# Kernel tuning notes

Measured on AMD Instinct MI355X. Metric: run time of the kernel, lower is better.

## Reference

```python
import jax, jax.numpy as jnp
import numpy as np

IN_CH = 128
OUT_CH = 256
KSIZE = 3
DOWN = 2
WSCALE_GAIN = 1.0
LR_MUL = 1.0
ACT_GAIN = float(np.sqrt(2.0))  # lrelu def_gain
CONV_CLAMP = 256.0
LRELU_SLOPE = 0.2


def _setup_filter():
    # upfirdn2d.setup_filter([1,3,3,1]): normalize 1D then outer product -> 2D
    f1 = jnp.asarray([1.0, 3.0, 3.0, 1.0], dtype=jnp.float32)
    f1 = f1 / jnp.sum(f1)
    f2 = jnp.outer(f1, f1)  # [4,4]
    return f2


def setup_inputs() -> dict:
    key = jax.random.key(0)
    k1, k2 = jax.random.split(key)
    x = jax.random.normal(k1, (16, IN_CH, 256, 256), dtype=jnp.float32)
    weight = jax.random.normal(k2, (OUT_CH, IN_CH, KSIZE, KSIZE), dtype=jnp.float32)
    bias = jnp.zeros((OUT_CH,), dtype=jnp.float32)
    return {"x": x, "weight": weight, "bias": bias}


def reference(x, weight, bias):
    # runtime_gain = 1.0
    fan_in = KSIZE * KSIZE * IN_CH
    wscale = WSCALE_GAIN / np.sqrt(fan_in) * LR_MUL  # use_wscale=True
    w = weight * jnp.float32(wscale)
    b = bias * jnp.float32(LR_MUL)

    # filter_padding for k=3, fh=fw=4, down=2 -> (2,2,2,2) as (left,right,top,bottom)
    pad = (KSIZE // 2 + (4 - DOWN + 1) // 2, KSIZE // 2 + (4 - DOWN) // 2)
    # upfirdn2d(x, f, down=1, padding): pad then correlate with flipped filter
    f2 = _setup_filter()
    f2 = f2[::-1, ::-1]  # flip (symmetric here, kept for faithfulness)
    C = x.shape[1]
    fk = jnp.broadcast_to(f2[None, None], (C, 1, 4, 4))  # depthwise kernel
    x = lax.pad_fn(x, pad) if False else jnp.pad(x, ((0, 0), (0, 0), (pad[1], pad[0]) if False else (pad[0], pad[1]), (pad[0], pad[1])))
    x = jax.lax.conv_general_dilated(
        x, fk, window_strides=(1, 1), padding='VALID',
        dimension_numbers=('NCHW', 'OIHW', 'NCHW'),
        feature_group_count=C)

    # strided conv2d, padding=0, stride=down
    x = jax.lax.conv_general_dilated(
        x, w, window_strides=(DOWN, DOWN), padding='VALID',
        dimension_numbers=('NCHW', 'OIHW', 'NCHW'))

    # fused bias + lrelu + gain + clamp
    x = x + b[None, :, None, None]
    x = jnp.where(x >= 0, x, x * jnp.float32(LRELU_SLOPE)) * jnp.float32(ACT_GAIN)
    x = jnp.clip(x, -jnp.float32(CONV_CLAMP), jnp.float32(CONV_CLAMP))
    return x
```

## Files before the change

### kernel.cpp

```cpp
#include <hip/hip_runtime.h>

typedef __attribute__((ext_vector_type(8))) short bf16x8;
typedef __attribute__((ext_vector_type(4))) float f32x4;
typedef __attribute__((ext_vector_type(2))) float f32x2;
typedef __attribute__((ext_vector_type(4))) unsigned int u32x4;

static __device__ __forceinline__ unsigned short f2bf(float f) {
    union { float f; unsigned u; } v; v.f = f;
    return (unsigned short)((v.u + 0x7FFFu + ((v.u >> 16) & 1u)) >> 16);
}

static __device__ __forceinline__ void g2l16(const void* g, void* l) {
    __builtin_amdgcn_global_load_lds(
        (const __attribute__((address_space(1))) unsigned int*)g,
        (__attribute__((address_space(3))) unsigned int*)l, 16, 0, 0);
}

__global__ void prep_weights(const float* __restrict__ w, unsigned short* __restrict__ wp) {
    int t = blockIdx.x * 256 + threadIdx.x;
    const float wscale = 0.02946278254943948f;
    int cw = t & 31;
    int oc = (t >> 5) & 255;
    int cr = t >> 13;
    int ch = cr / 9;
    int rs = cr - ch * 9;
    int r  = rs / 3;
    int s  = rs - r * 3;
    int c  = ch * 32 + cw;
    wp[t] = f2bf(w[((oc * 128 + c) * 3 + r) * 3 + s] * wscale);
}

#define BPX(ROW) {                                                             \
    int _xr = xr0 + (ROW);                                                     \
    int _xc = _xr < 0 ? 0 : (_xr > 255 ? 255 : _xr);                           \
    float _rm = (_xr == _xc) ? 0.125f : 0.0f;                                  \
    const float* _p0 = pq0 + (_xc << 8);                                       \
    const float* _p1 = pq1 + (_xc << 8);                                       \
    f32x4 _l0, _l1; f32x2 _h0, _h1;                                            \
    __builtin_memcpy(&_l0, _p0, 16); __builtin_memcpy(&_h0, _p0 + 4, 8);       \
    __builtin_memcpy(&_l1, _p1, 16); __builtin_memcpy(&_h1, _p1 + 4, 8);       \
    hA0[(ROW) & 3] = (_l0.x + 3.f * (_l0.y + _l0.z) + _l0.w) * _rm;            \
    hB0[(ROW) & 3] = (_l0.y + 3.f * (_l0.z + _l0.w) + _h0.x) * _rm;            \
    hC0[(ROW) & 3] = (_l0.z + 3.f * (_l0.w + _h0.x) + _h0.y) * _rm;            \
    hA1[(ROW) & 3] = (_l1.x + 3.f * (_l1.y + _l1.z) + _l1.w) * _rm;            \
    hB1[(ROW) & 3] = (_l1.y + 3.f * (_l1.z + _l1.w) + _h1.x) * _rm;            \
    hC1[(ROW) & 3] = (_l1.z + 3.f * (_l1.w + _h1.x) + _h1.y) * _rm;            \
}
#define BPS(ROW) {                                                             \
    int _xr = xr0 + (ROW);                                                     \
    float a0=0.f,a1=0.f,a2=0.f,a3=0.f,a4=0.f,a5=0.f;                           \
    float b0=0.f,b1=0.f,b2=0.f,b3=0.f,b4=0.f,b5=0.f;                           \
    if ((unsigned)_xr < 256u) {                                                \
        const float* _p0 = pq0 + (_xr << 8);                                   \
        const float* _p1 = pq1 + (_xr << 8);                                   \
        if ((unsigned)(wc + 0) < 256u) { a0 = _p0[0]; b0 = _p1[0]; }           \
        if ((unsigned)(wc + 1) < 256u) { a1 = _p0[1]; b1 = _p1[1]; }           \
        if ((unsigned)(wc + 2) < 256u) { a2 = _p0[2]; b2 = _p1[2]; }           \
        if ((unsigned)(wc + 3) < 256u) { a3 = _p0[3]; b3 = _p1[3]; }           \
        if ((unsigned)(wc + 4) < 256u) { a4 = _p0[4]; b4 = _p1[4]; }           \
        if ((unsigned)(wc + 5) < 256u) { a5 = _p0[5]; b5 = _p1[5]; }           \
    }                                                                          \
    hA0[(ROW) & 3] = (a0 + 3.f * (a1 + a2) + a3) * 0.125f;                     \
    hB0[(ROW) & 3] = (a1 + 3.f * (a2 + a3) + a4) * 0.125f;                     \
    hC0[(ROW) & 3] = (a2 + 3.f * (a3 + a4) + a5) * 0.125f;                     \
    hA1[(ROW) & 3] = (b0 + 3.f * (b1 + b2) + b3) * 0.125f;                     \
    hB1[(ROW) & 3] = (b1 + 3.f * (b2 + b3) + b4) * 0.125f;                     \
    hC1[(ROW) & 3] = (b2 + 3.f * (b3 + b4) + b5) * 0.125f;                     \
}
#define BPV(ROW) {                                                             \
    float vA0 = (hA0[(ROW-3)&3] + 3.f*(hA0[(ROW-2)&3]+hA0[(ROW-1)&3]) + hA0[(ROW)&3]) * 0.125f; \
    float vA1 = (hA1[(ROW-3)&3] + 3.f*(hA1[(ROW-2)&3]+hA1[(ROW-1)&3]) + hA1[(ROW)&3]) * 0.125f; \
    float vB0 = (hB0[(ROW-3)&3] + 3.f*(hB0[(ROW-2)&3]+hB0[(ROW-1)&3]) + hB0[(ROW)&3]) * 0.125f; \
    float vB1 = (hB1[(ROW-3)&3] + 3.f*(hB1[(ROW-2)&3]+hB1[(ROW-1)&3]) + hB1[(ROW)&3]) * 0.125f; \
    unsigned _rb = (unsigned)(ROW - 3) * 2112u;                                \
    *(unsigned*)(blds + _rb + o0) = (unsigned)f2bf(vA0) | ((unsigned)f2bf(vA1) << 16); \
    *(unsigned*)(blds + _rb + o1) = (unsigned)f2bf(vB0) | ((unsigned)f2bf(vB1) << 16); \
    if (a15) {                                                                 \
        float vC0 = (hC0[(ROW-3)&3] + 3.f*(hC0[(ROW-2)&3]+hC0[(ROW-1)&3]) + hC0[(ROW)&3]) * 0.125f; \
        float vC1 = (hC1[(ROW-3)&3] + 3.f*(hC1[(ROW-2)&3]+hC1[(ROW-1)&3]) + hC1[(ROW)&3]) * 0.125f; \
        *(unsigned*)(blds + _rb + o2) = (unsigned)f2bf(vC0) | ((unsigned)f2bf(vC1) << 16); \
    }                                                                          \
}
#define BPF(ROW) BPX(ROW) BPV(ROW)
#define BPP(ROW) BPS(ROW) BPV(ROW)

__global__ __launch_bounds__(256, 4)
void blur_rec(const float* __restrict__ x, unsigned char* __restrict__ bm) {
    __shared__ __align__(16) unsigned char blds[35904];
    const int bx   = blockIdx.x;
    const int cg   = bx & 3;
    const int tile = (bx >> 2) & 127;
    const int n    = bx >> 9;
    const int u0   = (tile >> 3) * 8;
    const int v0   = (tile & 7) * 16;
    const int tid  = threadIdx.x;
    const int a    = tid & 15;
    const int chp  = tid >> 4;
    const bool a15 = (a == 15);
    const int wc   = 2 * v0 - 2 + 2 * a;
    const bool edge = (v0 == 0 && a == 0) || (v0 == 112 && a15);
    const float* pq0 = x + (size_t)(n * 128 + cg * 32 + 2 * chp) * 65536 + wc;
    const float* pq1 = pq0 + 65536;
    const int xr0 = 2 * u0 - 2;

    const int J0 = 2 * a, J1 = 2 * a + 1;
    const unsigned cb2 = (unsigned)(chp & 3) * 4u;
    const unsigned o0 = (unsigned)((J0 ^ ((J0 >> 1) & 1)) * 64) + ((((unsigned)chp >> 2) ^ (((unsigned)J0 >> 2) & 3u)) << 4) + cb2;
    const unsigned o1 = (unsigned)((J1 ^ ((J1 >> 1) & 1)) * 64) + ((((unsigned)chp >> 2) ^ (((unsigned)J1 >> 2) & 3u)) << 4) + cb2;
    const unsigned o2 = 2048u + (((unsigned)chp >> 2) << 4) + cb2;

    {
        float hA0[4], hB0[4], hC0[4], hA1[4], hB1[4], hC1[4];
        if (!edge) {
            BPX(0) BPX(1) BPX(2)
            BPF(3)  BPF(4)  BPF(5)  BPF(6)  BPF(7)  BPF(8)  BPF(9)  BPF(10)
            BPF(11) BPF(12) BPF(13) BPF(14) BPF(15) BPF(16) BPF(17) BPF(18) BPF(19)
        } else {
            BPS(0) BPS(1) BPS(2)
            BPP(3)  BPP(4)  BPP(5)  BPP(6)  BPP(7)  BPP(8)  BPP(9)  BPP(10)
            BPP(11) BPP(12) BPP(13) BPP(14) BPP(15) BPP(16) BPP(17) BPP(18) BPP(19)
        }
    }
    __syncthreads();
    unsigned char* dst = bm + (size_t)bx * 35904u;
    #pragma unroll
    for (int k = 0; k < 8; ++k)
        *(u32x4*)(dst + (unsigned)(tid + 256 * k) * 16u) =
            *(const u32x4*)(blds + (unsigned)(tid + 256 * k) * 16u);
    if (tid < 196)
        *(u32x4*)(dst + (unsigned)(tid + 2048) * 16u) =
            *(const u32x4*)(blds + (unsigned)(tid + 2048) * 16u);
}

#define MF __builtin_amdgcn_mfma_f32_16x16x32_bf16
#define WLOAD2(S0, S1, KOFF) {                                                 \
    const unsigned short* _wn = wbase + (size_t)(KOFF) * 8192;                 \
    S0 = *(const bf16x8*)(_wn); S1 = *(const bf16x8*)(_wn + 512);              \
}
#define CSTEP8(BUF, ADRS, R, S0, S1) {                                         \
    const unsigned char* _ab = lds + (BUF) + (ADRS) + (R) * 2112;              \
    bf16x8 a0 = *(const bf16x8*)(_ab);                                         \
    bf16x8 a1 = *(const bf16x8*)(_ab +  4224);                                 \
    bf16x8 a2 = *(const bf16x8*)(_ab +  8448);                                 \
    bf16x8 a3 = *(const bf16x8*)(_ab + 12672);                                 \
    bf16x8 a4 = *(const bf16x8*)(_ab + 16896);                                 \
    bf16x8 a5 = *(const bf16x8*)(_ab + 21120);                                 \
    bf16x8 a6 = *(const bf16x8*)(_ab + 25344);                                 \
    bf16x8 a7 = *(const bf16x8*)(_ab + 29568);                                 \
    __builtin_amdgcn_s_setprio(1);                                             \
    acc[0][0]=MF(a0,S0,acc[0][0],0,0,0); acc[0][1]=MF(a0,S1,acc[0][1],0,0,0);  \
    acc[1][0]=MF(a1,S0,acc[1][0],0,0,0); acc[1][1]=MF(a1,S1,acc[1][1],0,0,0);  \
    acc[2][0]=MF(a2,S0,acc[2][0],0,0,0); acc[2][1]=MF(a2,S1,acc[2][1],0,0,0);  \
    acc[3][0]=MF(a3,S0,acc[3][0],0,0,0); acc[3][1]=MF(a3,S1,acc[3][1],0,0,0);  \
    acc[4][0]=MF(a4,S0,acc[4][0],0,0,0); acc[4][1]=MF(a4,S1,acc[4][1],0,0,0);  \
    acc[5][0]=MF(a5,S0,acc[5][0],0,0,0); acc[5][1]=MF(a5,S1,acc[5][1],0,0,0);  \
    acc[6][0]=MF(a6,S0,acc[6][0],0,0,0); acc[6][1]=MF(a6,S1,acc[6][1],0,0,0);  \
    acc[7][0]=MF(a7,S0,acc[7][0],0,0,0); acc[7][1]=MF(a7,S1,acc[7][1],0,0,0);  \
    __builtin_amdgcn_s_setprio(0);                                             \
}
#define CHUNK8(BUF, BASE, A0,A1, B0,B1)                                        \
    CSTEP8(BUF, adr0, 0, A0,A1) WLOAD2(A0,A1, (BASE)+2)                        \
    CSTEP8(BUF, adr1, 0, B0,B1) WLOAD2(B0,B1, (BASE)+3)                        \
    CSTEP8(BUF, adr2, 0, A0,A1) WLOAD2(A0,A1, (BASE)+4)                        \
    CSTEP8(BUF, adr0, 1, B0,B1) WLOAD2(B0,B1, (BASE)+5)                        \
    CSTEP8(BUF, adr1, 1, A0,A1) WLOAD2(A0,A1, (BASE)+6)                        \
    CSTEP8(BUF, adr2, 1, B0,B1) WLOAD2(B0,B1, (BASE)+7)                        \
    CSTEP8(BUF, adr0, 2, A0,A1) WLOAD2(A0,A1, (BASE)+8)                        \
    CSTEP8(BUF, adr1, 2, B0,B1) WLOAD2(B0,B1, (BASE)+9)                        \
    CSTEP8(BUF, adr2, 2, A0,A1) WLOAD2(A0,A1, (BASE)+10)
#define CHUNK8_LAST(BUF, BASE, A0,A1, B0,B1)                                   \
    CSTEP8(BUF, adr0, 0, A0,A1) WLOAD2(A0,A1, (BASE)+2)                        \
    CSTEP8(BUF, adr1, 0, B0,B1) WLOAD2(B0,B1, (BASE)+3)                        \
    CSTEP8(BUF, adr2, 0, A0,A1) WLOAD2(A0,A1, (BASE)+4)                        \
    CSTEP8(BUF, adr0, 1, B0,B1) WLOAD2(B0,B1, (BASE)+5)                        \
    CSTEP8(BUF, adr1, 1, A0,A1) WLOAD2(A0,A1, (BASE)+6)                        \
    CSTEP8(BUF, adr2, 1, B0,B1) WLOAD2(B0,B1, (BASE)+7)                        \
    CSTEP8(BUF, adr0, 2, A0,A1) WLOAD2(A0,A1, (BASE)+8)                        \
    CSTEP8(BUF, adr1, 2, B0,B1)                                                \
    CSTEP8(BUF, adr2, 2, A0,A1)

__global__ __launch_bounds__(512, 4)
void conv_stage2(const unsigned char* __restrict__ bm, const unsigned short* __restrict__ wp,
                 const float* __restrict__ bias, float* __restrict__ out) {
    __shared__ __align__(16) unsigned char lds[2 * 35904];

    const int bx = blockIdx.x;
    const int n  = bx >> 7;
    const int tt = bx & 127;
    const int u0 = (tt >> 3) * 8;
    const int v0 = (tt & 7) * 16;

    const int tid  = threadIdx.x;
    const int lane = tid & 63;
    const int wid  = tid >> 6;
    const int g    = lane >> 4;
    const int wq   = lane & 15;

    const unsigned char* rec = bm + (size_t)((n * 128 + tt) * 4) * 35904u;

#define STAGE(BUF, CG) {                                                       \
    const unsigned char* _src = rec + (size_t)(CG) * 35904u;                   \
    _Pragma("unroll")                                                          \
    for (int k = 0; k < 4; ++k)                                                \
        g2l16(_src + (unsigned)(tid + 512 * k) * 16u,                          \
              lds + (BUF) + (unsigned)(tid + 512 * k) * 16u);                  \
    if (tid < 196)                                                             \
        g2l16(_src + (unsigned)(tid + 2048) * 16u,                             \
              lds + (BUF) + (unsigned)(tid + 2048) * 16u);                     \
}

    unsigned adr0, adr1, adr2;
    {
        #pragma unroll
        for (int s = 0; s < 3; ++s) {
            unsigned bj = 2u * (unsigned)wq + (unsigned)s;
            unsigned av = (bj ^ ((bj >> 1) & 1u)) * 64u
                        + (((unsigned)g ^ ((bj >> 2) & 3u)) << 4);
            if (s == 0) adr0 = av; else if (s == 1) adr1 = av; else adr2 = av;
        }
    }

    const unsigned short* wbase = wp + (size_t)(wid * 32 + wq) * 32 + g * 8;
    bf16x8 WA0, WA1, WB0, WB1;
    WLOAD2(WA0, WA1, 0)
    WLOAD2(WB0, WB1, 1)

    f32x4 acc[8][2];
    #pragma unroll
    for (int i = 0; i < 8; ++i) {
        acc[i][0] = (f32x4){0.f, 0.f, 0.f, 0.f};
        acc[i][1] = (f32x4){0.f, 0.f, 0.f, 0.f};
    }

    STAGE(0, 0)
    __syncthreads();

    STAGE(35904, 1)
    CHUNK8(0, 0, WA0, WA1, WB0, WB1)
    __syncthreads();

    STAGE(0, 2)
    CHUNK8(35904, 9, WB0, WB1, WA0, WA1)
    __syncthreads();

    STAGE(35904, 3)
    CHUNK8(0, 18, WA0, WA1, WB0, WB1)
    __syncthreads();

    CHUNK8_LAST(35904, 27, WB0, WB1, WA0, WA1)

    const float gain = 1.4142135623730951f;
    #pragma unroll
    for (int nf = 0; nf < 2; ++nf) {
        const int ocg = wid * 32 + nf * 16 + wq;
        const float bb = bias[ocg];
        #pragma unroll
        for (int mf = 0; mf < 8; ++mf) {
            f32x4 o;
            #pragma unroll
            for (int i = 0; i < 4; ++i) {
                float z = acc[mf][nf][i] + bb;
                z = (z >= 0.f ? z : 0.2f * z) * gain;
                o[i] = fminf(fmaxf(z, -256.f), 256.f);
            }
            *(f32x4*)(out + (((size_t)n * 256 + ocg) * 128 + (u0 + mf)) * 128 + v0 + 4 * g) = o;
        }
    }
}

#define FROW(row) {                                                            \
    int xr  = xr0 + (row);                                                     \
    int xrc = xr < 0 ? 0 : (xr > 255 ? 255 : xr);                              \
    float rm = (xr == xrc) ? 0.125f : 0.0f;                                    \
    const float* p = q + (xrc << 8);                                           \
    f32x4 lo; f32x2 hi;                                                        \
    __builtin_memcpy(&lo, p, 16);                                              \
    __builtin_memcpy(&hi, p + 4, 8);                                           \
    hA[(row) & 3] = (lo.x + 3.f * (lo.y + lo.z) + lo.w) * rm;                  \
    hB[(row) & 3] = (lo.y + 3.f * (lo.z + lo.w) + hi.x) * rm;                  \
    hC[(row) & 3] = (lo.z + 3.f * (lo.w + hi.x) + hi.y) * rm;                  \
}
#define SROW(row) {                                                            \
    int xr = xr0 + (row);                                                      \
    float wv0=0.f,wv1=0.f,wv2=0.f,wv3=0.f,wv4=0.f,wv5=0.f;                     \
    if ((unsigned)xr < 256u) {                                                 \
        const float* p = q + (xr << 8);                                        \
        if ((unsigned)(wc + 0) < 256u) wv0 = p[0];                             \
        if ((unsigned)(wc + 1) < 256u) wv1 = p[1];                             \
        if ((unsigned)(wc + 2) < 256u) wv2 = p[2];                             \
        if ((unsigned)(wc + 3) < 256u) wv3 = p[3];                             \
        if ((unsigned)(wc + 4) < 256u) wv4 = p[4];                             \
        if ((unsigned)(wc + 5) < 256u) wv5 = p[5];                             \
    }                                                                          \
    hA[(row) & 3] = (wv0 + 3.f * (wv1 + wv2) + wv3) * 0.125f;                  \
    hB[(row) & 3] = (wv1 + 3.f * (wv2 + wv3) + wv4) * 0.125f;                  \
    hC[(row) & 3] = (wv2 + 3.f * (wv3 + wv4) + wv5) * 0.125f;                  \
}
#define VROW(row) {                                                            \
    float bv0 = (hA[(row - 3) & 3] + 3.f * (hA[(row - 2) & 3] + hA[(row - 1) & 3]) + hA[(row) & 3]) * 0.125f; \
    float bv1 = (hB[(row - 3) & 3] + 3.f * (hB[(row - 2) & 3] + hB[(row - 1) & 3]) + hB[(row) & 3]) * 0.125f; \
    unsigned rb = (unsigned)(row - 3) * 2640u;                                 \
    *(unsigned short*)(flds + rb + o0) = f2bf(bv0);                            \
    *(unsigned short*)(flds + rb + o1) = f2bf(bv1);                            \
    if (a == 15) {                                                             \
        float bv2 = (hC[(row - 3) & 3] + 3.f * (hC[(row - 2) & 3] + hC[(row - 1) & 3]) + hC[(row) & 3]) * 0.125f; \
        *(unsigned short*)(flds + rb + o2) = f2bf(bv2);                        \
    }                                                                          \
}
__global__ __launch_bounds__(512, 4)
void conv_blur_mfma(const float* __restrict__ x, const unsigned short* __restrict__ wp,
                    const float* __restrict__ bias, float* __restrict__ out) {
    __shared__ __align__(16) unsigned char flds[17 * 33 * 80];
    const int bx = blockIdx.x;
    const int n  = bx >> 7;
    const int tt = bx & 127;
    const int u0 = (tt >> 3) * 8;
    const int v0 = (tt & 7) * 16;
    const int tid  = threadIdx.x;
    const int lane = tid & 63;
    const int wid  = tid >> 6;
    const int wm   = wid >> 2;
    const int wn   = wid & 3;
    const int g    = lane >> 4;
    const int wq   = lane & 15;
    const int a   = tid & 15;
    const int chl = tid >> 4;
    const int wc  = 2 * v0 - 2 + 2 * a;
    const bool edge = (v0 == 0 && a == 0) || (v0 == 112 && a == 15);
    const float* planeBase = x + (size_t)(n * 128 + chl) * 65536;
    const int xr0 = 2 * u0 - 2;
    const unsigned chpart = (unsigned)(((chl >> 1) & 3) * 4 + (chl & 1) * 2);
    const unsigned q4 = (unsigned)(chl >> 3);
    const int c0 = 2 * a;
    const unsigned o0 = (unsigned)(c0 + 0) * 80u + ((q4 ^ (((unsigned)(c0 + 0) >> 3) & 3u)) << 4) + chpart;
    const unsigned o1 = (unsigned)(c0 + 1) * 80u + ((q4 ^ (((unsigned)(c0 + 1) >> 3) & 3u)) << 4) + chpart;
    const unsigned o2 = (unsigned)(c0 + 2) * 80u + ((q4 ^ (((unsigned)(c0 + 2) >> 3) & 3u)) << 4) + chpart;
    const unsigned short* wpL = wp + (size_t)(wn * 64 + wq) * 32 + g * 8;
    f32x4 acc[4][4];
    #pragma unroll
    for (int i = 0; i < 4; ++i)
        #pragma unroll
        for (int j = 0; j < 4; ++j)
            acc[i][j] = (f32x4){0.f, 0.f, 0.f, 0.f};
    for (int ch = 0; ch < 4; ++ch) {
        const float* q = planeBase + (size_t)ch * 32 * 65536 + wc;
        float hA[4], hB[4], hC[4];
        if (!edge) { FROW(0) FROW(1) FROW(2) }
        else       { SROW(0) SROW(1) SROW(2) }
        __syncthreads();
        if (!edge) {
            #pragma unroll
            for (int row = 3; row < 20; ++row) { FROW(row) VROW(row) }
        } else {
            #pragma unroll
            for (int row = 3; row < 20; ++row) { SROW(row) VROW(row) }
        }
        __syncthreads();
        const unsigned short* wpc = wpL + (size_t)ch * 9 * 8192;
        #pragma unroll 1
        for (int r = 0; r < 3; ++r) {
            #pragma unroll 1
            for (int s = 0; s < 3; ++s) {
                bf16x8 b0 = *(const bf16x8*)(wpc + 0 * 512);
                bf16x8 b1 = *(const bf16x8*)(wpc + 1 * 512);
                bf16x8 b2 = *(const bf16x8*)(wpc + 2 * 512);
                bf16x8 b3 = *(const bf16x8*)(wpc + 3 * 512);
                wpc += 8192;
                int bj = 2 * wq + s;
                unsigned cb = (unsigned)bj * 80u + ((unsigned)(g ^ ((bj >> 3) & 3)) << 4);
                #pragma unroll
                for (int mf = 0; mf < 4; ++mf) {
                    int bi = 2 * (wm * 4 + mf) + r;
                    bf16x8 afrag = *(const bf16x8*)(flds + (unsigned)bi * 2640u + cb);
                    acc[mf][0] = MF(afrag, b0, acc[mf][0], 0, 0, 0);
                    acc[mf][1] = MF(afrag, b1, acc[mf][1], 0, 0, 0);
                    acc[mf][2] = MF(afrag, b2, acc[mf][2], 0, 0, 0);
                    acc[mf][3] = MF(afrag, b3, acc[mf][3], 0, 0, 0);
                }
            }
        }
    }
    const float gain = 1.4142135623730951f;
    #pragma unroll
    for (int nf = 0; nf < 4; ++nf) {
        int ocg = wn * 64 + nf * 16 + wq;
        float bv = bias[ocg];
        #pragma unroll
        for (int mf = 0; mf < 4; ++mf) {
            int u = u0 + wm * 4 + mf;
            f32x4 o;
            #pragma unroll
            for (int i = 0; i < 4; ++i) {
                float z = acc[mf][nf][i] + bv;
                z = (z >= 0.f ? z : 0.2f * z) * gain;
                o[i] = fminf(fmaxf(z, -256.f), 256.f);
            }
            *(f32x4*)(out + (((size_t)n * 256 + ocg) * 128 + u) * 128 + v0 + 4 * g) = o;
        }
    }
}

extern "C" void kernel_launch(void* const* d_in, const int* in_sizes, int n_in,
                              void* d_out, int out_size, void* d_ws, size_t ws_size,
                              hipStream_t stream) {
    const float* x    = (const float*)d_in[0];
    const float* w    = (const float*)d_in[1];
    const float* bias = (const float*)d_in[2];
    unsigned short* wp = (unsigned short*)d_ws;
    float* out = (float*)d_out;

    const size_t BM_BYTES = (size_t)8192 * 35904u;
    const size_t NEED = 589824u + BM_BYTES;
    prep_weights<<<1152, 256, 0, stream>>>(w, wp);
    if (ws_size >= NEED) {
        unsigned char* bm = (unsigned char*)d_ws + 589824;
        blur_rec<<<8192, 256, 0, stream>>>(x, bm);
        conv_stage2<<<2048, 512, 0, stream>>>(bm, wp, bias, out);
    } else {
        conv_blur_mfma<<<2048, 512, 0, stream>>>(x, wp, bias, out);
    }
}
```

Baseline: 476.7 us.

## Split blur staging into two LDS halves, unify edge path, swizzle block order

The blur kernel now stages its 17 output rows in two passes through a 9-row LDS buffer instead of one 17-row buffer. This cuts shared memory per block and raises the launch-bounds occupancy hint from 4 to 6. The separate scalar edge path is replaced by clamped vector loads with select-based zeroing. Block indices are also remapped so consecutive workgroups spread across batches and tiles. The cost is an extra barrier and copy phase, and the remap changes cache locality.

```diff
diff --git a/kernel.cpp b/kernel.cpp
--- a/kernel.cpp
+++ b/kernel.cpp
@@ -30,49 +30,38 @@
     wp[t] = f2bf(w[((oc * 128 + c) * 3 + r) * 3 + s] * wscale);
 }
 
-#define BPX(ROW) {                                                             \
+#define BRW(ROW) {                                                             \
     int _xr = xr0 + (ROW);                                                     \
     int _xc = _xr < 0 ? 0 : (_xr > 255 ? 255 : _xr);                           \
     float _rm = (_xr == _xc) ? 0.125f : 0.0f;                                  \
-    const float* _p0 = pq0 + (_xc << 8);                                       \
-    const float* _p1 = pq1 + (_xc << 8);                                       \
+    const float* _q0 = p0lo + (_xc << 8);                                      \
+    const float* _h0p = p0hi + (_xc << 8);                                     \
+    const float* _q1 = p1lo + (_xc << 8);                                      \
+    const float* _h1p = p1hi + (_xc << 8);                                     \
     f32x4 _l0, _l1; f32x2 _h0, _h1;                                            \
-    __builtin_memcpy(&_l0, _p0, 16); __builtin_memcpy(&_h0, _p0 + 4, 8);       \
-    __builtin_memcpy(&_l1, _p1, 16); __builtin_memcpy(&_h1, _p1 + 4, 8);       \
-    hA0[(ROW) & 3] = (_l0.x + 3.f * (_l0.y + _l0.z) + _l0.w) * _rm;            \
-    hB0[(ROW) & 3] = (_l0.y + 3.f * (_l0.z + _l0.w) + _h0.x) * _rm;            \
-    hC0[(ROW) & 3] = (_l0.z + 3.f * (_l0.w + _h0.x) + _h0.y) * _rm;            \
-    hA1[(ROW) & 3] = (_l1.x + 3.f * (_l1.y + _l1.z) + _l1.w) * _rm;            \
-    hB1[(ROW) & 3] = (_l1.y + 3.f * (_l1.z + _l1.w) + _h1.x) * _rm;            \
-    hC1[(ROW) & 3] = (_l1.z + 3.f * (_l1.w + _h1.x) + _h1.y) * _rm;            \
-}
-#define BPS(ROW) {                                                             \
-    int _xr = xr0 + (ROW);                                                     \
-    float a0=0.f,a1=0.f,a2=0.f,a3=0.f,a4=0.f,a5=0.f;                           \
-    float b0=0.f,b1=0.f,b2=0.f,b3=0.f,b4=0.f,b5=0.f;                           \
-    if ((unsigned)_xr < 256u) {                                                \
-        const float* _p0 = pq0 + (_xr << 8);                                   \
-        const float* _p1 = pq1 + (_xr << 8);                                   \
-        if ((unsigned)(wc + 0) < 256u) { a0 = _p0[0]; b0 = _p1[0]; }           \
-        if ((unsigned)(wc + 1) < 256u) { a1 = _p0[1]; b1 = _p1[1]; }           \
-        if ((unsigned)(wc + 2) < 256u) { a2 = _p0[2]; b2 = _p1[2]; }           \
-        if ((unsigned)(wc + 3) < 256u) { a3 = _p0[3]; b3 = _p1[3]; }           \
-        if ((unsigned)(wc + 4) < 256u) { a4 = _p0[4]; b4 = _p1[4]; }           \
-        if ((unsigned)(wc + 5) < 256u) { a5 = _p0[5]; b5 = _p1[5]; }           \
-    }                                                                          \
-    hA0[(ROW) & 3] = (a0 + 3.f * (a1 + a2) + a3) * 0.125f;                     \
-    hB0[(ROW) & 3] = (a1 + 3.f * (a2 + a3) + a4) * 0.125f;                     \
-    hC0[(ROW) & 3] = (a2 + 3.f * (a3 + a4) + a5) * 0.125f;                     \
-    hA1[(ROW) & 3] = (b0 + 3.f * (b1 + b2) + b3) * 0.125f;                     \
-    hB1[(ROW) & 3] = (b1 + 3.f * (b2 + b3) + b4) * 0.125f;                     \
-    hC1[(ROW) & 3] = (b2 + 3.f * (b3 + b4) + b5) * 0.125f;                     \
-}
-#define BPV(ROW) {                                                             \
+    __builtin_memcpy(&_l0, _q0, 16); __builtin_memcpy(&_h0, _h0p, 8);          \
+    __builtin_memcpy(&_l1, _q1, 16); __builtin_memcpy(&_h1, _h1p, 8);          \
+    float w00 = eL ? 0.f : _l0.x,  w01 = eL ? 0.f : _l0.y;                     \
+    float w02 = eL ? _l0.x : _l0.z, w03 = eL ? _l0.y : _l0.w;                  \
+    float w04 = eR ? 0.f : (eL ? _l0.z : _h0.x);                               \
+    float w05 = eR ? 0.f : (eL ? _l0.w : _h0.y);                               \
+    float w10 = eL ? 0.f : _l1.x,  w11 = eL ? 0.f : _l1.y;                     \
+    float w12 = eL ? _l1.x : _l1.z, w13 = eL ? _l1.y : _l1.w;                  \
+    float w14 = eR ? 0.f : (eL ? _l1.z : _h1.x);                               \
+    float w15 = eR ? 0.f : (eL ? _l1.w : _h1.y);                               \
+    hA0[(ROW) & 3] = (w00 + 3.f * (w01 + w02) + w03) * _rm;                    \
+    hB0[(ROW) & 3] = (w01 + 3.f * (w02 + w03) + w04) * _rm;                    \
+    hC0[(ROW) & 3] = (w02 + 3.f * (w03 + w04) + w05) * _rm;                    \
+    hA1[(ROW) & 3] = (w10 + 3.f * (w11 + w12) + w13) * _rm;                    \
+    hB1[(ROW) & 3] = (w11 + 3.f * (w12 + w13) + w14) * _rm;                    \
+    hC1[(ROW) & 3] = (w12 + 3.f * (w13 + w14) + w15) * _rm;                    \
+}
+#define BWV(ROW, LBASE) {                                                      \
     float vA0 = (hA0[(ROW-3)&3] + 3.f*(hA0[(ROW-2)&3]+hA0[(ROW-1)&3]) + hA0[(ROW)&3]) * 0.125f; \
     float vA1 = (hA1[(ROW-3)&3] + 3.f*(hA1[(ROW-2)&3]+hA1[(ROW-1)&3]) + hA1[(ROW)&3]) * 0.125f; \
     float vB0 = (hB0[(ROW-3)&3] + 3.f*(hB0[(ROW-2)&3]+hB0[(ROW-1)&3]) + hB0[(ROW)&3]) * 0.125f; \
     float vB1 = (hB1[(ROW-3)&3] + 3.f*(hB1[(ROW-2)&3]+hB1[(ROW-1)&3]) + hB1[(ROW)&3]) * 0.125f; \
-    unsigned _rb = (unsigned)(ROW - 3) * 2112u;                                \
+    unsigned _rb = (unsigned)(LBASE) * 2112u;                                  \
     *(unsigned*)(blds + _rb + o0) = (unsigned)f2bf(vA0) | ((unsigned)f2bf(vA1) << 16); \
     *(unsigned*)(blds + _rb + o1) = (unsigned)f2bf(vB0) | ((unsigned)f2bf(vB1) << 16); \
     if (a15) {                                                                 \
@@ -81,13 +70,13 @@
         *(unsigned*)(blds + _rb + o2) = (unsigned)f2bf(vC0) | ((unsigned)f2bf(vC1) << 16); \
     }                                                                          \
 }
-#define BPF(ROW) BPX(ROW) BPV(ROW)
-#define BPP(ROW) BPS(ROW) BPV(ROW)
-
-__global__ __launch_bounds__(256, 4)
+
+__global__ __launch_bounds__(256, 6)
 void blur_rec(const float* __restrict__ x, unsigned char* __restrict__ bm) {
-    __shared__ __align__(16) unsigned char blds[35904];
-    const int bx   = blockIdx.x;
+    __shared__ __align__(16) unsigned char blds[9 * 2112];
+
+    const int braw = blockIdx.x;
+    const int bx   = ((braw & 7) << 10) | (braw >> 3);
     const int cg   = bx & 3;
     const int tile = (bx >> 2) & 127;
     const int n    = bx >> 9;
@@ -98,38 +87,51 @@
     const int chp  = tid >> 4;
     const bool a15 = (a == 15);
     const int wc   = 2 * v0 - 2 + 2 * a;
-    const bool edge = (v0 == 0 && a == 0) || (v0 == 112 && a15);
-    const float* pq0 = x + (size_t)(n * 128 + cg * 32 + 2 * chp) * 65536 + wc;
-    const float* pq1 = pq0 + 65536;
+    const bool eL  = (v0 == 0 && a == 0);
+    const bool eR  = (v0 == 112 && a15);
+    const int colLo = eL ? 0 : wc;
+    const int colHi = eR ? 248 : (wc + 4);
+    const float* plane0 = x + (size_t)(n * 128 + cg * 32 + 2 * chp) * 65536;
+    const float* p0lo = plane0 + colLo;
+    const float* p0hi = plane0 + colHi;
+    const float* p1lo = p0lo + 65536;
+    const float* p1hi = p0hi + 65536;
     const int xr0 = 2 * u0 - 2;
 
     const int J0 = 2 * a, J1 = 2 * a + 1;
     const unsigned cb2 = (unsigned)(chp & 3) * 4u;
-    const unsigned o0 = (unsigned)((J0 ^ ((J0 >> 1) & 1)) * 64) + ((((unsigned)chp >> 2) ^ (((unsigned)J0 >> 2) & 3u)) << 4) + cb2;
-    const unsigned o1 = (unsigned)((J1 ^ ((J1 >> 1) & 1)) * 64) + ((((unsigned)chp >> 2) ^ (((unsigned)J1 >> 2) & 3u)) << 4) + cb2;
+    const unsigned o0 = (unsigned)((J0 ^ ((J0 >> 1) & 1)) * 64)
+                      + ((((unsigned)chp >> 2) ^ (((unsigned)J0 >> 2) & 3u)) << 4) + cb2;
+    const unsigned o1 = (unsigned)((J1 ^ ((J1 >> 1) & 1)) * 64)
+                      + ((((unsigned)chp >> 2) ^ (((unsigned)J1 >> 2) & 3u)) << 4) + cb2;
     const unsigned o2 = 2048u + (((unsigned)chp >> 2) << 4) + cb2;
 
-    {
-        float hA0[4], hB0[4], hC0[4], hA1[4], hB1[4], hC1[4];
-        if (!edge) {
-            BPX(0) BPX(1) BPX(2)
-            BPF(3)  BPF(4)  BPF(5)  BPF(6)  BPF(7)  BPF(8)  BPF(9)  BPF(10)
-            BPF(11) BPF(12) BPF(13) BPF(14) BPF(15) BPF(16) BPF(17) BPF(18) BPF(19)
-        } else {
-            BPS(0) BPS(1) BPS(2)
-            BPP(3)  BPP(4)  BPP(5)  BPP(6)  BPP(7)  BPP(8)  BPP(9)  BPP(10)
-            BPP(11) BPP(12) BPP(13) BPP(14) BPP(15) BPP(16) BPP(17) BPP(18) BPP(19)
-        }
-    }
-    __syncthreads();
     unsigned char* dst = bm + (size_t)bx * 35904u;
-    #pragma unroll
-    for (int k = 0; k < 8; ++k)
-        *(u32x4*)(dst + (unsigned)(tid + 256 * k) * 16u) =
-            *(const u32x4*)(blds + (unsigned)(tid + 256 * k) * 16u);
-    if (tid < 196)
-        *(u32x4*)(dst + (unsigned)(tid + 2048) * 16u) =
-            *(const u32x4*)(blds + (unsigned)(tid + 2048) * 16u);
+    float hA0[4], hB0[4], hC0[4], hA1[4], hB1[4], hC1[4];
+
+    BRW(0) BRW(1) BRW(2)
+    BRW(3)  BWV(3, 0)   BRW(4)  BWV(4, 1)   BRW(5)  BWV(5, 2)
+    BRW(6)  BWV(6, 3)   BRW(7)  BWV(7, 4)   BRW(8)  BWV(8, 5)
+    BRW(9)  BWV(9, 6)   BRW(10) BWV(10, 7)  BRW(11) BWV(11, 8)
+    __syncthreads();
+    #pragma unroll
+    for (int k = 0; k < 5; ++k) {
+        int sl = tid + 256 * k;
+        if (sl < 1188)
+            *(u32x4*)(dst + (unsigned)sl * 16u) = *(const u32x4*)(blds + (unsigned)sl * 16u);
+    }
+    __syncthreads();
+    BRW(12) BWV(12, 0)  BRW(13) BWV(13, 1)  BRW(14) BWV(14, 2)
+    BRW(15) BWV(15, 3)  BRW(16) BWV(16, 4)  BRW(17) BWV(17, 5)
+    BRW(18) BWV(18, 6)  BRW(19) BWV(19, 7)
+    __syncthreads();
+    unsigned char* dst2 = dst + 19008u;
+    #pragma unroll
+    for (int k = 0; k < 5; ++k) {
+        int sl = tid + 256 * k;
+        if (sl < 1056)
+            *(u32x4*)(dst2 + (unsigned)sl * 16u) = *(const u32x4*)(blds + (unsigned)sl * 16u);
+    }
 }
 
 #define MF __builtin_amdgcn_mfma_f32_16x16x32_bf16
```

Result: faster. 413.5 us (-13.3%).
